# Kernel optimization log

Hardware: AMD Instinct MI355X
Metric: run time of the kernel (lower is better)

The kernel has to match this reference:

```python
import jax, jax.numpy as jnp
import numpy as np

N_NODES = 50000
N_EDGES = 800000
N_GRAPHS = 128
F_IN = 128
HID = 64
EDGE_DIM = 16
H1, H2 = 4, 2
NEG_SLOPE = 0.2


def _glorot(key, shape, fan_in):
    return jax.random.normal(key, shape, dtype=jnp.float32) / np.sqrt(fan_in)


def setup_inputs() -> dict:
    key = jax.random.key(0)
    ks = jax.random.split(key, 20)
    x = jax.random.normal(ks[0], (N_NODES, F_IN), dtype=jnp.float32)
    edge_attr = jax.random.normal(ks[1], (N_EDGES, EDGE_DIM), dtype=jnp.float32)
    edge_index = jax.random.randint(ks[2], (2, N_EDGES), 0, N_NODES, dtype=jnp.int32)
    # evenly spread graph ids so every graph is non-empty (sorted)
    batch = (jnp.arange(N_NODES, dtype=jnp.int32) * N_GRAPHS) // N_NODES
    p = {
        'W1': _glorot(ks[3], (F_IN, H1 * HID), F_IN),
        'a_src1': _glorot(ks[4], (H1, HID), HID),
        'a_dst1': _glorot(ks[5], (H1, HID), HID),
        'We1': _glorot(ks[6], (EDGE_DIM, H1 * HID), EDGE_DIM),
        'a_e1': _glorot(ks[7], (H1, HID), HID),
        'b1': jnp.zeros((H1 * HID,), jnp.float32),
        'W2': _glorot(ks[8], (H1 * HID, H2 * HID), H1 * HID),
        'a_src2': _glorot(ks[9], (H2, HID), HID),
        'a_dst2': _glorot(ks[10], (H2, HID), HID),
        'We2': _glorot(ks[11], (EDGE_DIM, H2 * HID), EDGE_DIM),
        'a_e2': _glorot(ks[12], (H2, HID), HID),
        'b2': jnp.zeros((HID,), jnp.float32),
        'Wr': _glorot(ks[13], (HID, 1), HID),
        'br': jnp.zeros((1,), jnp.float32),
    }
    return dict(x=x, edge_attr=edge_attr, edge_index=edge_index, batch=batch, **p)


def _segment_softmax(scores, seg, num_segments):
    # scores: [E, H], softmax grouped by seg (destination node)
    m = jax.ops.segment_max(scores, seg, num_segments)
    m = jnp.where(jnp.isfinite(m), m, 0.0)
    ex = jnp.exp(scores - m[seg])
    s = jax.ops.segment_sum(ex, seg, num_segments)
    return ex / (s[seg] + 1e-16)


def _add_self_loops(edge_index, edge_attr, n):
    # PyG add_self_loops with fill_value='mean': per-dst mean of edge_attr
    src, dst = edge_index[0], edge_index[1]
    cnt = jax.ops.segment_sum(jnp.ones((src.shape[0],), jnp.float32), dst, n)
    loop_attr = jax.ops.segment_sum(edge_attr, dst, n) / jnp.maximum(cnt, 1.0)[:, None]
    loop = jnp.arange(n, dtype=src.dtype)
    return (jnp.concatenate([src, loop]), jnp.concatenate([dst, loop]),
            jnp.concatenate([edge_attr, loop_attr], axis=0))


def _gat_layer(x, e_attr, src, dst, W, a_src, a_dst, We, a_e, b, heads, outc, concat):
    n = x.shape[0]
    xs = (x @ W).reshape(n, heads, outc)                 # [N,H,C]
    s_src = jnp.einsum('nhc,hc->nh', xs, a_src)
    s_dst = jnp.einsum('nhc,hc->nh', xs, a_dst)
    ee = (e_attr @ We).reshape(-1, heads, outc)          # [E,H,C]
    s_e = jnp.einsum('ehc,hc->eh', ee, a_e)
    score = jax.nn.leaky_relu(s_src[src] + s_dst[dst] + s_e, NEG_SLOPE)  # [E,H]
    alpha = _segment_softmax(score, dst, n)
    out = jax.ops.segment_sum(xs[src] * alpha[..., None], dst, n)        # [N,H,C]
    out = out.reshape(n, heads * outc) if concat else out.mean(axis=1)
    return out + b


def reference(x, edge_attr, edge_index, batch,
              W1, a_src1, a_dst1, We1, a_e1, b1,
              W2, a_src2, a_dst2, We2, a_e2, b2, Wr, br):
    n = x.shape[0]
    src, dst, ea = _add_self_loops(edge_index, edge_attr, n)
    h = _gat_layer(x, ea, src, dst, W1, a_src1, a_dst1, We1, a_e1, b1, H1, HID, True)
    h = jax.nn.relu(h)
    h = _gat_layer(h, ea, src, dst, W2, a_src2, a_dst2, We2, a_e2, b2, H2, HID, False)
    g = jax.ops.segment_max(h, batch, N_GRAPHS)          # global max pool [G, HID]
    return g @ Wr + br
```

## Files before the change

### kernel.cpp

```cpp
#include <hip/hip_runtime.h>
#include <hip/hip_bf16.h>

#define DEVINL __device__ __forceinline__
typedef __hip_bfloat16 bf16;

typedef __attribute__((ext_vector_type(8))) __bf16 bf16x8;
typedef __attribute__((ext_vector_type(4))) float f32x4;

static constexpr int N_NODES  = 50000;
static constexpr int N_EDGES  = 800000;
static constexpr int N_GRAPHS = 128;
static constexpr float NEG_SLOPE = 0.2f;

DEVINL float ldIn(const void* __restrict__ p, size_t i, int isbf) {
    if (isbf) return __bfloat162float(((const bf16*)p)[i]);
    return ((const float*)p)[i];
}

DEVINL unsigned short f2bf(float f) {
    bf16 b = __float2bfloat16(f);
    return *reinterpret_cast<unsigned short*>(&b);
}

DEVINL float bfu2f(unsigned short u) {
    return __uint_as_float(((unsigned)u) << 16);
}

template<int H>
DEVINL void ldrow(const unsigned short* __restrict__ p, unsigned short (&v)[H]) {
    if (H == 4) *reinterpret_cast<uint2*>(v)    = *reinterpret_cast<const uint2*>(p);
    else        *reinterpret_cast<unsigned*>(v) = *reinterpret_cast<const unsigned*>(p);
}

DEVINL float lrelu_exp(float sc) {
    sc = sc > 0.f ? sc : NEG_SLOPE * sc;
    return __expf(sc);
}

__global__ void detect_dtype_kernel(const unsigned short* __restrict__ xu,
                                    int* __restrict__ flag)
{
    int t = threadIdx.x;
    int bad = 0;
    for (int i = t; i < 1024; i += 64) {
        unsigned u = xu[2 * i];
        float v = __uint_as_float(u << 16);
        if (!(fabsf(v) <= 1e4f)) bad = 1;
    }
    unsigned long long m = __ballot(bad);
    if (t == 0) *flag = m ? 0 : 1;
}

__global__ void build_M_kernel(const void* __restrict__ We1, const void* __restrict__ ae1,
                               const void* __restrict__ We2, const void* __restrict__ ae2,
                               const int* __restrict__ flagp,
                               float* __restrict__ M1, float* __restrict__ M2)
{
    const int isbf = *flagp;
    int t = threadIdx.x;
    if (t < 64) {
        int d = t >> 2, h = t & 3;
        float s = 0.f;
        for (int c = 0; c < 64; ++c)
            s += ldIn(We1, d * 256 + h * 64 + c, isbf) * ldIn(ae1, h * 64 + c, isbf);
        M1[d * 4 + h] = s;
    }
    if (t < 32) {
        int d = t >> 1, h = t & 1;
        float s = 0.f;
        for (int c = 0; c < 64; ++c)
            s += ldIn(We2, d * 128 + h * 64 + c, isbf) * ldIn(ae2, h * 64 + c, isbf);
        M2[d * 2 + h] = s;
    }
}

template<int K, int M>
__global__ void build_wfrag_kernel(const void* __restrict__ W, const int* __restrict__ flagp,
                                   bf16* __restrict__ Wfrag)
{
    constexpr int KS = K / 32;
    const int isbf = *flagp;
    int idx = blockIdx.x * 256 + threadIdx.x;
    constexpr int total = (M / 16) * KS * 64 * 8;
    if (idx >= total) return;
    int j    = idx & 7;
    int lane = (idx >> 3) & 63;
    int rem  = idx >> 9;
    int ks   = rem % KS;
    int ct   = rem / KS;
    int k = ks * 32 + (lane >> 4) * 8 + j;
    int n = ct * 16 + (lane & 15);
    Wfrag[idx] = __float2bfloat16(ldIn(W, (size_t)k * M + n, isbf));
}

template<int K, int M, int AMODE>
__global__ __launch_bounds__(256)
void gemm_mfma_kernel(const void* __restrict__ A, const bf16* __restrict__ Wfrag,
                      bf16* __restrict__ C, const int* __restrict__ flagp, int N)
{
    constexpr int KS = K / 32, CT = M / 16;
    constexpr int LDA = K + 8;
    __shared__ __align__(16) unsigned short Asm[64 * LDA];
    const int isbf = *flagp;
    const int tid  = threadIdx.x;
    const int wave = tid >> 6, lane = tid & 63;
    const int n0 = blockIdx.x * 64;

    for (int i = tid; i < 64 * (K / 8); i += 256) {
        int r  = i / (K / 8);
        int kc = (i % (K / 8)) * 8;
        int n  = n0 + r;
        unsigned short v[8] = {0, 0, 0, 0, 0, 0, 0, 0};
        if (n < N) {
            size_t base = (size_t)n * K + kc;
            if (AMODE == 1 || isbf) {
                *reinterpret_cast<uint4*>(v) =
                    *reinterpret_cast<const uint4*>((const unsigned short*)A + base);
            } else {
                const float* Af = (const float*)A + base;
                float4 f0 = *reinterpret_cast<const float4*>(Af);
                float4 f1 = *reinterpret_cast<const float4*>(Af + 4);
                v[0] = f2bf(f0.x); v[1] = f2bf(f0.y); v[2] = f2bf(f0.z); v[3] = f2bf(f0.w);
                v[4] = f2bf(f1.x); v[5] = f2bf(f1.y); v[6] = f2bf(f1.z); v[7] = f2bf(f1.w);
            }
        }
        *reinterpret_cast<uint4*>(&Asm[r * LDA + kc]) = *reinterpret_cast<uint4*>(v);
    }
    __syncthreads();

    f32x4 acc[CT];
    #pragma unroll
    for (int ct = 0; ct < CT; ++ct) acc[ct] = (f32x4){0.f, 0.f, 0.f, 0.f};

    const int arow  = wave * 16 + (lane & 15);
    const int akoff = (lane >> 4) * 8;
    #pragma unroll
    for (int ks = 0; ks < KS; ++ks) {
        bf16x8 af = *reinterpret_cast<const bf16x8*>(&Asm[arow * LDA + ks * 32 + akoff]);
        #pragma unroll
        for (int ct = 0; ct < CT; ++ct) {
            bf16x8 bfr = *reinterpret_cast<const bf16x8*>(
                &Wfrag[(((size_t)ct * KS + ks) * 64 + lane) * 8]);
            acc[ct] = __builtin_amdgcn_mfma_f32_16x16x32_bf16(af, bfr, acc[ct], 0, 0, 0);
        }
    }

    const int crow0 = n0 + wave * 16 + (lane >> 4) * 4;
    const int ccol  = lane & 15;
    #pragma unroll
    for (int ct = 0; ct < CT; ++ct) {
        #pragma unroll
        for (int r = 0; r < 4; ++r) {
            int row = crow0 + r;
            if (row < N) C[(size_t)row * M + ct * 16 + ccol] = __float2bfloat16(acc[ct][r]);
        }
    }
}

__global__ void csr_count_kernel(const int* __restrict__ dst, int* __restrict__ cnt)
{
    int e = blockIdx.x * blockDim.x + threadIdx.x;
    if (e >= N_EDGES) return;
    atomicAdd(&cnt[dst[e]], 1);
}

__global__ __launch_bounds__(256)
void scan_sum_kernel(const int* __restrict__ cnt, int* __restrict__ bsum)
{
    __shared__ int sm[256];
    int i = blockIdx.x * 256 + threadIdx.x;
    sm[threadIdx.x] = (i < N_NODES) ? cnt[i] : 0;
    __syncthreads();
    for (int off = 128; off; off >>= 1) {
        if (threadIdx.x < off) sm[threadIdx.x] += sm[threadIdx.x + off];
        __syncthreads();
    }
    if (threadIdx.x == 0) bsum[blockIdx.x] = sm[0];
}

__global__ __launch_bounds__(256)
void scan_off_kernel(int* __restrict__ bsum, int nb)
{
    __shared__ int sm[256];
    int tid = threadIdx.x;
    int v = (tid < nb) ? bsum[tid] : 0;
    sm[tid] = v;
    __syncthreads();
    for (int off = 1; off < 256; off <<= 1) {
        int t = (tid >= off) ? sm[tid - off] : 0;
        __syncthreads();
        sm[tid] += t;
        __syncthreads();
    }
    if (tid < nb) bsum[tid] = sm[tid] - v;
}

__global__ __launch_bounds__(256)
void scan_final_kernel(const int* __restrict__ cnt, const int* __restrict__ bsum,
                       int* __restrict__ row, int* __restrict__ cursor)
{
    __shared__ int sm[256];
    int i = blockIdx.x * 256 + threadIdx.x;
    int tid = threadIdx.x;
    int v = (i < N_NODES) ? cnt[i] : 0;
    sm[tid] = v;
    __syncthreads();
    for (int off = 1; off < 256; off <<= 1) {
        int t = (tid >= off) ? sm[tid - off] : 0;
        __syncthreads();
        sm[tid] += t;
        __syncthreads();
    }
    int excl = sm[tid] - v + bsum[blockIdx.x];
    if (i < N_NODES) { row[i] = excl; cursor[i] = excl; }
    if (i == N_NODES - 1) row[N_NODES] = excl + v;
}

__global__ void csr_scatter_kernel(const int* __restrict__ srcI, const int* __restrict__ dstI,
                                   const void* __restrict__ eattr, const int* __restrict__ flagp,
                                   const float* __restrict__ M1, const float* __restrict__ M2,
                                   int* __restrict__ cursor, int* __restrict__ srcS,
                                   float* __restrict__ se1, float* __restrict__ se2)
{
    const int isbf = *flagp;
    int e = blockIdx.x * blockDim.x + threadIdx.x;
    if (e >= N_EDGES) return;
    float attr[16];
    #pragma unroll
    for (int k = 0; k < 16; ++k) attr[k] = ldIn(eattr, (size_t)e * 16 + k, isbf);
    float4 o1 = {0.f, 0.f, 0.f, 0.f};
    float2 o2 = {0.f, 0.f};
    #pragma unroll
    for (int k = 0; k < 16; ++k) {
        o1.x += attr[k] * M1[k * 4 + 0];
        o1.y += attr[k] * M1[k * 4 + 1];
        o1.z += attr[k] * M1[k * 4 + 2];
        o1.w += attr[k] * M1[k * 4 + 3];
        o2.x += attr[k] * M2[k * 2 + 0];
        o2.y += attr[k] * M2[k * 2 + 1];
    }
    int d = dstI[e];
    int pos = atomicAdd(&cursor[d], 1);
    srcS[pos] = srcI[e];
    *reinterpret_cast<float4*>(&se1[(size_t)pos * 4]) = o1;
    *reinterpret_cast<float2*>(&se2[(size_t)pos * 2]) = o2;
}

template<int H>
__global__ __launch_bounds__(256)
void node_scores_kernel(const bf16* __restrict__ xs, const void* __restrict__ a_src,
                        const void* __restrict__ a_dst, const int* __restrict__ flagp,
                        float* __restrict__ sA, float* __restrict__ sD)
{
    const int isbf = *flagp;
    int wave = (blockIdx.x * 256 + threadIdx.x) >> 6;
    int lane = threadIdx.x & 63;
    if (wave >= N_NODES) return;
    #pragma unroll
    for (int h = 0; h < H; ++h) {
        float v  = __bfloat162float(xs[(size_t)wave * (H * 64) + h * 64 + lane]);
        float ps = v * ldIn(a_src, h * 64 + lane, isbf);
        float pd = v * ldIn(a_dst, h * 64 + lane, isbf);
        for (int off = 32; off; off >>= 1) {
            ps += __shfl_down(ps, off);
            pd += __shfl_down(pd, off);
        }
        if (lane == 0) { sA[wave * H + h] = ps; sD[wave * H + h] = pd; }
    }
}

template<int H, int LAYER>
__global__ __launch_bounds__(256)
void agg_fused_kernel(const int* __restrict__ row, const int* __restrict__ srcS,
                      const bf16* __restrict__ xs, const float* __restrict__ seE,
                      const float* __restrict__ sA, const float* __restrict__ sD,
                      const void* __restrict__ bias,
                      const int* __restrict__ flagp, void* __restrict__ out)
{
    const int isbf = *flagp;
    int dv = (blockIdx.x * 256 + threadIdx.x) >> 6;
    const int d = __builtin_amdgcn_readfirstlane(dv);
    const int lane = threadIdx.x & 63;
    if (d >= N_NODES) return;
    const int h = (lane * H) >> 6;
    const unsigned short* xsu = (const unsigned short*)xs;
    const float sDv = sD[(size_t)d * H + h];
    const float sAd = sA[(size_t)d * H + h];

    float acc[H];
    #pragma unroll
    for (int i = 0; i < H; ++i) acc[i] = 0.f;
    float den = 0.f, seSum = 0.f;

    const int b = row[d], eend = row[d + 1];
    int j = b;
    for (; j + 7 < eend; j += 8) {
        int s[8];
        float se[8], sa[8];
        unsigned short v[8][H];
        #pragma unroll
        for (int u = 0; u < 8; ++u) s[u] = srcS[j + u];
        #pragma unroll
        for (int u = 0; u < 8; ++u) se[u] = seE[(size_t)(j + u) * H + h];
        #pragma unroll
        for (int u = 0; u < 8; ++u) sa[u] = sA[(size_t)s[u] * H + h];
        #pragma unroll
        for (int u = 0; u < 8; ++u) ldrow<H>(&xsu[(size_t)s[u] * (H * 64) + lane * H], v[u]);
        #pragma unroll
        for (int u = 0; u < 8; ++u) {
            float w = lrelu_exp(sa[u] + sDv + se[u]);
            seSum += se[u];
            den += w;
            #pragma unroll
            for (int i = 0; i < H; ++i) acc[i] += w * bfu2f(v[u][i]);
        }
    }
    for (; j < eend; ++j) {
        const int s = srcS[j];
        const float se = seE[(size_t)j * H + h];
        const float sa = sA[(size_t)s * H + h];
        unsigned short v[H];
        ldrow<H>(&xsu[(size_t)s * (H * 64) + lane * H], v);
        const float w = lrelu_exp(sa + sDv + se);
        seSum += se;
        den += w;
        #pragma unroll
        for (int i = 0; i < H; ++i) acc[i] += w * bfu2f(v[i]);
    }

    {
        const int cntv = eend - b;
        const float seM = seSum / fmaxf((float)cntv, 1.f);
        const float wS = lrelu_exp(sAd + sDv + seM);
        unsigned short v[H];
        ldrow<H>(&xsu[(size_t)d * (H * 64) + lane * H], v);
        den += wS;
        #pragma unroll
        for (int i = 0; i < H; ++i) acc[i] += wS * bfu2f(v[i]);
    }

    const float rden = 1.f / (den + 1e-16f);
    if (LAYER == 1) {
        unsigned short o[H];
        #pragma unroll
        for (int i = 0; i < H; ++i) {
            float v = acc[i] * rden + ldIn(bias, lane * H + i, isbf);
            o[i] = f2bf(v > 0.f ? v : 0.f);
        }
        *reinterpret_cast<uint2*>(&((unsigned short*)out)[(size_t)d * (H * 64) + lane * H]) =
            *reinterpret_cast<uint2*>(o);
    } else {
        float v0 = acc[0] * rden, v1 = acc[1] * rden;
        float p0 = __shfl(v0, lane + 32), p1 = __shfl(v1, lane + 32);
        if (lane < 32) {
            float2 o;
            o.x = 0.5f * (v0 + p0) + ldIn(bias, lane * 2 + 0, isbf);
            o.y = 0.5f * (v1 + p1) + ldIn(bias, lane * 2 + 1, isbf);
            *reinterpret_cast<float2*>(&((float*)out)[(size_t)d * 64 + lane * 2]) = o;
        }
    }
}

__global__ __launch_bounds__(256)
void pool_max_kernel(const float* __restrict__ h2, const int* __restrict__ batch,
                     float* __restrict__ g)
{
    int gi = blockIdx.x;
    int lo = 0, hi = N_NODES;
    while (lo < hi) { int mid = (lo + hi) >> 1; if (batch[mid] < gi) lo = mid + 1; else hi = mid; }
    int start = lo;
    lo = start; hi = N_NODES;
    while (lo < hi) { int mid = (lo + hi) >> 1; if (batch[mid] < gi + 1) lo = mid + 1; else hi = mid; }
    int end = lo;
    int c = threadIdx.x & 63, chunk = threadIdx.x >> 6;
    float m = -INFINITY;
    for (int n = start + chunk; n < end; n += 4) m = fmaxf(m, h2[(size_t)n * 64 + c]);
    __shared__ float sm[256];
    sm[threadIdx.x] = m;
    __syncthreads();
    if (threadIdx.x < 64) {
        m = fmaxf(fmaxf(sm[threadIdx.x], sm[threadIdx.x + 64]),
                  fmaxf(sm[threadIdx.x + 128], sm[threadIdx.x + 192]));
        g[gi * 64 + threadIdx.x] = m;
    }
}

__global__ void readout_kernel(const float* __restrict__ g, const void* __restrict__ Wr,
                               const void* __restrict__ br, const int* __restrict__ flagp,
                               void* __restrict__ out)
{
    const int isbf = *flagp;
    int gi = blockIdx.x;
    int lane = threadIdx.x;
    float p = g[gi * 64 + lane] * ldIn(Wr, lane, isbf);
    for (int off = 32; off; off >>= 1) p += __shfl_down(p, off);
    if (lane == 0) {
        float r = p + ldIn(br, 0, isbf);
        if (isbf) ((bf16*)out)[gi] = __float2bfloat16(r);
        else      ((float*)out)[gi] = r;
    }
}

extern "C" void kernel_launch(void* const* d_in, const int* in_sizes, int n_in,
                              void* d_out, int out_size, void* d_ws, size_t ws_size,
                              hipStream_t stream)
{
    const void* x     = d_in[0];
    const void* ea    = d_in[1];
    const int*  eidx  = (const int*)d_in[2];
    const int*  batch = (const int*)d_in[3];
    const void* W1  = d_in[4];
    const void* as1 = d_in[5];
    const void* ad1 = d_in[6];
    const void* We1 = d_in[7];
    const void* ae1 = d_in[8];
    const void* b1  = d_in[9];
    const void* W2  = d_in[10];
    const void* as2 = d_in[11];
    const void* ad2 = d_in[12];
    const void* We2 = d_in[13];
    const void* ae2 = d_in[14];
    const void* b2  = d_in[15];
    const void* Wr  = d_in[16];
    const void* br  = d_in[17];

    const int* srcI = eidx;
    const int* dstI = eidx + N_EDGES;

    float* ws    = (float*)d_ws;
    bf16*  xs    = (bf16*)ws;
    bf16*  h1    = (bf16*)(ws + 6400000);
    float* h2    = ws + 6400000;
    float* se1   = ws + 12800000;
    float* se2   = ws + 16000000;
    float* sA1   = ws + 17600000;
    float* sD1   = ws + 17800000;
    float* sA2   = ws + 18000000;
    float* sD2   = ws + 18100000;
    int*   ib    = (int*)(ws + 18200000);
    int*   row    = ib;
    int*   cursor = ib + 50016;
    int*   cnt    = ib + 100032;
    int*   bsum   = ib + 150048;
    int*   srcS   = ib + 150400;
    float* misc  = ws + 18200000 + 950400;
    int*   flag  = (int*)misc;
    float* M1    = misc + 16;
    float* M2    = misc + 80;
    float* gpool = misc + 112;
    bf16*  wf1   = (bf16*)(misc + 8320);
    bf16*  wf2   = (bf16*)(misc + 8320 + 16384);

    hipMemsetAsync(cnt, 0, N_NODES * sizeof(int), stream);

    detect_dtype_kernel<<<1, 64, 0, stream>>>((const unsigned short*)x, flag);
    build_M_kernel<<<1, 64, 0, stream>>>(We1, ae1, We2, ae2, flag, M1, M2);
    build_wfrag_kernel<128, 256><<<128, 256, 0, stream>>>(W1, flag, wf1);
    build_wfrag_kernel<256, 128><<<128, 256, 0, stream>>>(W2, flag, wf2);

    const int NB = (N_NODES + 255) / 256;
    csr_count_kernel<<<(N_EDGES + 255) / 256, 256, 0, stream>>>(dstI, cnt);
    scan_sum_kernel<<<NB, 256, 0, stream>>>(cnt, bsum);
    scan_off_kernel<<<1, 256, 0, stream>>>(bsum, NB);
    scan_final_kernel<<<NB, 256, 0, stream>>>(cnt, bsum, row, cursor);
    csr_scatter_kernel<<<(N_EDGES + 255) / 256, 256, 0, stream>>>(
        srcI, dstI, ea, flag, M1, M2, cursor, srcS, se1, se2);

    const int GB = (N_NODES + 63) / 64;

    gemm_mfma_kernel<128, 256, 0><<<GB, 256, 0, stream>>>(x, wf1, xs, flag, N_NODES);
    node_scores_kernel<4><<<(N_NODES + 3) / 4, 256, 0, stream>>>(xs, as1, ad1, flag, sA1, sD1);
    agg_fused_kernel<4, 1><<<(N_NODES + 3) / 4, 256, 0, stream>>>(
        row, srcS, xs, se1, sA1, sD1, b1, flag, h1);

    gemm_mfma_kernel<256, 128, 1><<<GB, 256, 0, stream>>>(h1, wf2, xs, flag, N_NODES);
    node_scores_kernel<2><<<(N_NODES + 3) / 4, 256, 0, stream>>>(xs, as2, ad2, flag, sA2, sD2);
    agg_fused_kernel<2, 2><<<(N_NODES + 3) / 4, 256, 0, stream>>>(
        row, srcS, xs, se2, sA2, sD2, b2, flag, h2);

    pool_max_kernel<<<N_GRAPHS, 256, 0, stream>>>(h2, batch, gpool);
    readout_kernel<<<N_GRAPHS, 64, 0, stream>>>(gpool, Wr, br, flag, d_out);
}
```

Baseline: 481.1 us.

## Fuse node score reduction into GEMM epilogue and pack edge records

Computes the per-node source/destination attention scores inside the MFMA GEMM epilogue from the fp32 accumulators, removing the separate node_scores kernels and their re-read of xs. Packs each sorted edge's source index and both layers' edge scores (as fp16) into one 16-byte record, so the aggregation kernels do a single vector load per edge instead of separate index and score loads. Edge scores lose precision from fp32 to fp16, and the score reduction now uses unrounded accumulators rather than bf16-stored xs, which slightly changes numerics.

```diff
diff --git a/kernel.cpp b/kernel.cpp
--- a/kernel.cpp
+++ b/kernel.cpp
@@ -1,5 +1,6 @@
 #include <hip/hip_runtime.h>
 #include <hip/hip_bf16.h>
+#include <hip/hip_fp16.h>
 
 #define DEVINL __device__ __forceinline__
 typedef __hip_bfloat16 bf16;
@@ -24,6 +25,17 @@
 
 DEVINL float bfu2f(unsigned short u) {
     return __uint_as_float(((unsigned)u) << 16);
+}
+
+DEVINL unsigned f2hbits(float f) {
+    __half h = __float2half(f);
+    return (unsigned)*reinterpret_cast<unsigned short*>(&h);
+}
+
+DEVINL float hbits2f(unsigned bits) {
+    unsigned short us = (unsigned short)bits;
+    __half h = *reinterpret_cast<__half*>(&us);
+    return __half2float(h);
 }
 
 template<int H>
@@ -93,10 +105,12 @@
     Wfrag[idx] = __float2bfloat16(ldIn(W, (size_t)k * M + n, isbf));
 }
 
-template<int K, int M, int AMODE>
+template<int K, int M, int AMODE, int H>
 __global__ __launch_bounds__(256)
 void gemm_mfma_kernel(const void* __restrict__ A, const bf16* __restrict__ Wfrag,
-                      bf16* __restrict__ C, const int* __restrict__ flagp, int N)
+                      bf16* __restrict__ C, const int* __restrict__ flagp, int N,
+                      const void* __restrict__ a_src, const void* __restrict__ a_dst,
+                      float* __restrict__ sA, float* __restrict__ sD)
 {
     constexpr int KS = K / 32, CT = M / 16;
     constexpr int LDA = K + 8;
@@ -155,6 +169,46 @@
             if (row < N) C[(size_t)row * M + ct * 16 + ccol] = __float2bfloat16(acc[ct][r]);
         }
     }
+
+    float psA[4][H], psD[4][H];
+    #pragma unroll
+    for (int r = 0; r < 4; ++r)
+        #pragma unroll
+        for (int hh = 0; hh < H; ++hh) { psA[r][hh] = 0.f; psD[r][hh] = 0.f; }
+    #pragma unroll
+    for (int ct = 0; ct < CT; ++ct) {
+        float as = ldIn(a_src, ct * 16 + ccol, isbf);
+        float ad = ldIn(a_dst, ct * 16 + ccol, isbf);
+        const int hh = ct >> 2;
+        #pragma unroll
+        for (int r = 0; r < 4; ++r) {
+            psA[r][hh] += acc[ct][r] * as;
+            psD[r][hh] += acc[ct][r] * ad;
+        }
+    }
+    #pragma unroll
+    for (int m = 1; m < 16; m <<= 1) {
+        #pragma unroll
+        for (int r = 0; r < 4; ++r)
+            #pragma unroll
+            for (int hh = 0; hh < H; ++hh) {
+                psA[r][hh] += __shfl_xor(psA[r][hh], m);
+                psD[r][hh] += __shfl_xor(psD[r][hh], m);
+            }
+    }
+    if (ccol == 0) {
+        #pragma unroll
+        for (int r = 0; r < 4; ++r) {
+            int row = crow0 + r;
+            if (row < N) {
+                #pragma unroll
+                for (int hh = 0; hh < H; ++hh) {
+                    sA[(size_t)row * H + hh] = psA[r][hh];
+                    sD[(size_t)row * H + hh] = psD[r][hh];
+                }
+            }
+        }
+    }
 }
 
 __global__ void csr_count_kernel(const int* __restrict__ dst, int* __restrict__ cnt)
@@ -219,8 +273,7 @@
 __global__ void csr_scatter_kernel(const int* __restrict__ srcI, const int* __restrict__ dstI,
                                    const void* __restrict__ eattr, const int* __restrict__ flagp,
                                    const float* __restrict__ M1, const float* __restrict__ M2,
-                                   int* __restrict__ cursor, int* __restrict__ srcS,
-                                   float* __restrict__ se1, float* __restrict__ se2)
+                                   int* __restrict__ cursor, uint4* __restrict__ erec)
 {
     const int isbf = *flagp;
     int e = blockIdx.x * blockDim.x + threadIdx.x;
@@ -241,38 +294,18 @@
     }
     int d = dstI[e];
     int pos = atomicAdd(&cursor[d], 1);
-    srcS[pos] = srcI[e];
-    *reinterpret_cast<float4*>(&se1[(size_t)pos * 4]) = o1;
-    *reinterpret_cast<float2*>(&se2[(size_t)pos * 2]) = o2;
-}
-
-template<int H>
-__global__ __launch_bounds__(256)
-void node_scores_kernel(const bf16* __restrict__ xs, const void* __restrict__ a_src,
-                        const void* __restrict__ a_dst, const int* __restrict__ flagp,
-                        float* __restrict__ sA, float* __restrict__ sD)
-{
-    const int isbf = *flagp;
-    int wave = (blockIdx.x * 256 + threadIdx.x) >> 6;
-    int lane = threadIdx.x & 63;
-    if (wave >= N_NODES) return;
-    #pragma unroll
-    for (int h = 0; h < H; ++h) {
-        float v  = __bfloat162float(xs[(size_t)wave * (H * 64) + h * 64 + lane]);
-        float ps = v * ldIn(a_src, h * 64 + lane, isbf);
-        float pd = v * ldIn(a_dst, h * 64 + lane, isbf);
-        for (int off = 32; off; off >>= 1) {
-            ps += __shfl_down(ps, off);
-            pd += __shfl_down(pd, off);
-        }
-        if (lane == 0) { sA[wave * H + h] = ps; sD[wave * H + h] = pd; }
-    }
+    uint4 rec;
+    rec.x = (unsigned)srcI[e];
+    rec.y = f2hbits(o1.x) | (f2hbits(o1.y) << 16);
+    rec.z = f2hbits(o1.z) | (f2hbits(o1.w) << 16);
+    rec.w = f2hbits(o2.x) | (f2hbits(o2.y) << 16);
+    erec[pos] = rec;
 }
 
 template<int H, int LAYER>
 __global__ __launch_bounds__(256)
-void agg_fused_kernel(const int* __restrict__ row, const int* __restrict__ srcS,
-                      const bf16* __restrict__ xs, const float* __restrict__ seE,
+void agg_fused_kernel(const int* __restrict__ row, const uint4* __restrict__ erec,
+                      const bf16* __restrict__ xs,
                       const float* __restrict__ sA, const float* __restrict__ sD,
                       const void* __restrict__ bias,
                       const int* __restrict__ flagp, void* __restrict__ out)
@@ -299,9 +332,16 @@
         float se[8], sa[8];
         unsigned short v[8][H];
         #pragma unroll
-        for (int u = 0; u < 8; ++u) s[u] = srcS[j + u];
-        #pragma unroll
-        for (int u = 0; u < 8; ++u) se[u] = seE[(size_t)(j + u) * H + h];
+        for (int u = 0; u < 8; ++u) {
+            uint4 rv = erec[j + u];
+            s[u] = (int)rv.x;
+            if (H == 4) {
+                unsigned w16 = (h & 2) ? rv.z : rv.y;
+                se[u] = hbits2f((h & 1) ? (w16 >> 16) : (w16 & 0xffffu));
+            } else {
+                se[u] = hbits2f(h ? (rv.w >> 16) : (rv.w & 0xffffu));
+            }
+        }
         #pragma unroll
         for (int u = 0; u < 8; ++u) sa[u] = sA[(size_t)s[u] * H + h];
         #pragma unroll
@@ -316,8 +356,15 @@
         }
     }
     for (; j < eend; ++j) {
-        const int s = srcS[j];
-        const float se = seE[(size_t)j * H + h];
+        uint4 rv = erec[j];
+        const int s = (int)rv.x;
+        float se;
+        if (H == 4) {
+            unsigned w16 = (h & 2) ? rv.z : rv.y;
+            se = hbits2f((h & 1) ? (w16 >> 16) : (w16 & 0xffffu));
+        } else {
+            se = hbits2f(h ? (rv.w >> 16) : (rv.w & 0xffffu));
+        }
         const float sa = sA[(size_t)s * H + h];
         unsigned short v[H];
         ldrow<H>(&xsu[(size_t)s * (H * 64) + lane * H], v);
@@ -431,19 +478,17 @@
     bf16*  xs    = (bf16*)ws;
     bf16*  h1    = (bf16*)(ws + 6400000);
     float* h2    = ws + 6400000;
-    float* se1   = ws + 12800000;
-    float* se2   = ws + 16000000;
-    float* sA1   = ws + 17600000;
-    float* sD1   = ws + 17800000;
-    float* sA2   = ws + 18000000;
-    float* sD2   = ws + 18100000;
-    int*   ib    = (int*)(ws + 18200000);
+    uint4* erec  = (uint4*)(ws + 12800000);
+    float* sA1   = ws + 16000000;
+    float* sD1   = ws + 16200000;
+    float* sA2   = ws + 16400000;
+    float* sD2   = ws + 16500000;
+    int*   ib    = (int*)(ws + 16600000);
     int*   row    = ib;
     int*   cursor = ib + 50016;
     int*   cnt    = ib + 100032;
     int*   bsum   = ib + 150048;
-    int*   srcS   = ib + 150400;
-    float* misc  = ws + 18200000 + 950400;
+    float* misc  = ws + 16600000 + 150400;
     int*   flag  = (int*)misc;
     float* M1    = misc + 16;
     float* M2    = misc + 80;
@@ -464,19 +509,19 @@
     scan_off_kernel<<<1, 256, 0, stream>>>(bsum, NB);
     scan_final_kernel<<<NB, 256, 0, stream>>>(cnt, bsum, row, cursor);
     csr_scatter_kernel<<<(N_EDGES + 255) / 256, 256, 0, stream>>>(
-        srcI, dstI, ea, flag, M1, M2, cursor, srcS, se1, se2);
+        srcI, dstI, ea, flag, M1, M2, cursor, erec);
 
     const int GB = (N_NODES + 63) / 64;
 
-    gemm_mfma_kernel<128, 256, 0><<<GB, 256, 0, stream>>>(x, wf1, xs, flag, N_NODES);
-    node_scores_kernel<4><<<(N_NODES + 3) / 4, 256, 0, stream>>>(xs, as1, ad1, flag, sA1, sD1);
+    gemm_mfma_kernel<128, 256, 0, 4><<<GB, 256, 0, stream>>>(
+        x, wf1, xs, flag, N_NODES, as1, ad1, sA1, sD1);
     agg_fused_kernel<4, 1><<<(N_NODES + 3) / 4, 256, 0, stream>>>(
-        row, srcS, xs, se1, sA1, sD1, b1, flag, h1);
-
-    gemm_mfma_kernel<256, 128, 1><<<GB, 256, 0, stream>>>(h1, wf2, xs, flag, N_NODES);
-    node_scores_kernel<2><<<(N_NODES + 3) / 4, 256, 0, stream>>>(xs, as2, ad2, flag, sA2, sD2);
+        row, erec, xs, sA1, sD1, b1, flag, h1);
+
+    gemm_mfma_kernel<256, 128, 1, 2><<<GB, 256, 0, stream>>>(
+        h1, wf2, xs, flag, N_NODES, as2, ad2, sA2, sD2);
     agg_fused_kernel<2, 2><<<(N_NODES + 3) / 4, 256, 0, stream>>>(
-        row, srcS, xs, se2, sA2, sD2, b2, flag, h2);
+        row, erec, xs, sA2, sD2, b2, flag, h2);
 
     pool_max_kernel<<<N_GRAPHS, 256, 0, stream>>>(h2, batch, gpool);
     readout_kernel<<<N_GRAPHS, 64, 0, stream>>>(gpool, Wr, br, flag, d_out);
```

Measured after the change: 429.9 us. 1.12x faster.
